# Kernel optimization log

Measured on AMD Instinct MI355X. Metric: run time of the kernel, lower is better.

The kernel has to match this reference:

```python
import jax, jax.numpy as jnp
import numpy as np

B, N, D, K = 16, 65536, 24, 512
ATTRACTION_WEIGHT = 1.0
REPULSION_WEIGHT = 1.5
MARGIN_WEIGHT = 5.0
THRESHOLD = 0.5
MARGIN = 0.2
TAU = 0.7


def setup_inputs() -> dict:
    key = jax.random.key(0)
    k1, k2, k3 = jax.random.split(key, 3)
    beta = jax.random.normal(k1, (B, N, 1), jnp.float32)
    embed = jax.random.normal(k2, (B, N, D), jnp.float32)
    # First K hits of each event are the condensation points (one per instance),
    # remaining hits get a random instance id in [0, K).
    rand_sid = jax.random.randint(k3, (B, N - K), 0, K, jnp.int32)
    cp_sid = jnp.broadcast_to(jnp.arange(K, dtype=jnp.int32), (B, K))
    slice_id = jnp.concatenate([cp_sid, rand_sid], axis=1)
    is_cp = jnp.concatenate(
        [jnp.ones((B, K), jnp.int32), jnp.zeros((B, N - K), jnp.int32)], axis=1)
    return {"beta": beta, "embed": embed, "slice_id": slice_id, "is_cp": is_cp}


def _per_batch(beta_b, emb_b, sid, cp):
    # beta_b: [N], emb_b: [N, D], sid: [N] int, cp: [N] int
    n = beta_b.shape[0]
    f32 = beta_b.dtype
    cp_mask = cp == 1
    pos_count = cp_mask.sum()
    neg_count = n - pos_count

    seg_cnt = jax.ops.segment_sum(jnp.ones((n,), f32), sid, num_segments=K)
    inst_present = seg_cnt > 0
    cp_per_inst = jax.ops.segment_sum(cp_mask.astype(f32), sid, num_segments=K)
    valid_inst = inst_present & (cp_per_inst == 1)  # inst_cp.sum() == 1

    # --- grouped softmax CE over each instance (temperature TAU) ---
    logits = jnp.clip(beta_b, -20.0, 20.0) / TAU
    seg_max = jax.ops.segment_max(logits, sid, num_segments=K)
    safe_max = jnp.where(inst_present, seg_max, 0.0)
    ex = jnp.exp(logits - safe_max[sid])
    denom = jax.ops.segment_sum(ex, sid, num_segments=K)
    cp_logit = jax.ops.segment_sum(jnp.where(cp_mask, logits, 0.0), sid,
                                   num_segments=K)  # exactly one cp when valid
    p_cp = jnp.exp(cp_logit - safe_max) / jnp.maximum(denom, 1e-30)
    loss_inst = -jnp.log(p_cp + 1e-9)
    slice_count = valid_inst.sum()
    beta_slice_ce = jnp.where(valid_inst, loss_inst, 0.0).sum() / jnp.maximum(slice_count, 1)

    # --- margin loss on sigmoid(beta) ---
    beta_prob = jax.nn.sigmoid(jnp.clip(beta_b, -20.0, 20.0))
    pos_m = jnp.where(cp_mask, jax.nn.relu(THRESHOLD + MARGIN - beta_prob), 0.0).sum() \
        / jnp.maximum(pos_count, 1)
    neg_m = jnp.where(cp_mask, 0.0, jax.nn.relu(beta_prob - (THRESHOLD - MARGIN))).sum() \
        / jnp.maximum(neg_count, 1)
    beta_loss = beta_slice_ce + MARGIN_WEIGHT * (pos_m + neg_m)

    # --- attraction: hits pulled to first CP of their instance ---
    idx = jnp.arange(n, dtype=jnp.int32)
    first_cp = jax.ops.segment_min(jnp.where(cp_mask, idx, n), sid, num_segments=K)
    has_cp = (first_cp < n) & inst_present
    cp_emb = emb_b[jnp.minimum(first_cp, n - 1)]  # [K, D]
    d2 = jnp.minimum(((emb_b - cp_emb[sid]) ** 2).sum(-1), 50.0)
    d2_mean = jax.ops.segment_sum(d2, sid, num_segments=K) / jnp.maximum(seg_cnt, 1.0)
    attraction = ATTRACTION_WEIGHT * jnp.where(has_cp, d2_mean, 0.0).sum()

    # --- repulsion: pairwise exp(-d2) between CP embeddings (incl. diagonal) ---
    m = has_cp.astype(f32)
    mcount = m.sum()
    sq = (cp_emb ** 2).sum(-1)
    pd2 = sq[:, None] + sq[None, :] - 2.0 * (cp_emb @ cp_emb.T)
    pd2 = jnp.clip(pd2, 0.0, 50.0)
    rep = (jnp.exp(-pd2) * (m[:, None] * m[None, :])).sum() / jnp.maximum(mcount * mcount, 1.0)
    repulsion = jnp.where(mcount > 1, REPULSION_WEIGHT * rep, 0.0)

    valid = (pos_count >= 1) & (neg_count >= 1) & (slice_count > 0)
    total = beta_loss + attraction + repulsion
    return total, beta_loss, attraction, repulsion, valid


def reference(beta, embed, slice_id, is_cp):
    beta = jnp.nan_to_num(jnp.squeeze(beta, -1), nan=0.0, posinf=0.0, neginf=0.0)
    embed = jnp.nan_to_num(embed, nan=0.0, posinf=0.0, neginf=0.0)
    total, bl, al, rl, valid = jax.vmap(_per_batch)(beta, embed, slice_id, is_cp)
    v = valid.astype(beta.dtype)
    count = v.sum()
    safe = jnp.maximum(count, 1.0)
    ok = count > 0
    final = jnp.where(ok, (total * v).sum() / safe, 0.0)
    beta_log = jnp.where(ok, (bl * v).sum() / safe, 0.0)
    attr_log = jnp.where(ok, (al * v).sum() / safe, 0.0)
    repl_log = jnp.where(ok, (rl * v).sum() / safe, 0.0)
    return final, beta_log, attr_log, repl_log
```

## Files before the change

kernel.cpp:

```cpp
#include <hip/hip_runtime.h>
#include <math.h>

#define BB 16
#define NN 65536
#define DD 24
#define KK 512
#define CH 64
#define HPB (NN / CH)
#define TPB 256
#define RPB 8
#define FIRST_INIT 0x7F7F7F7F

__device__ __forceinline__ float fixnum(float v) {
  return __builtin_isfinite(v) ? v : 0.0f;
}

__device__ __forceinline__ float blockReduceSum(float v, float* sbuf) {
  __syncthreads();
  #pragma unroll
  for (int off = 32; off > 0; off >>= 1) v += __shfl_down(v, off, 64);
  int wid = threadIdx.x >> 6, lane = threadIdx.x & 63;
  if (lane == 0) sbuf[wid] = v;
  __syncthreads();
  return sbuf[0] + sbuf[1] + sbuf[2] + sbuf[3];
}

__global__ __launch_bounds__(TPB) void k1_seg(
    const float* __restrict__ beta, const int* __restrict__ sid,
    const int* __restrict__ iscp,
    float* __restrict__ cnt_g, float* __restrict__ den_g,
    float* __restrict__ cpc_g, float* __restrict__ cpl_g,
    int* __restrict__ first_g, float* __restrict__ marg_g)
{
  __shared__ float s_cnt[KK], s_den[KK], s_cpc[KK], s_cpl[KK];
  __shared__ int   s_first[KK];
  __shared__ float sred[4];
  int b = blockIdx.x >> 6, c = blockIdx.x & 63, t = threadIdx.x;
  for (int k = t; k < KK; k += TPB) {
    s_cnt[k] = 0.f; s_den[k] = 0.f; s_cpc[k] = 0.f; s_cpl[k] = 0.f; s_first[k] = NN;
  }
  __syncthreads();
  int h0 = c * HPB + t * 4;
  size_t g0 = (size_t)b * NN + h0;
  float4 bv = *(const float4*)(beta + g0);
  int4   sv = *(const int4*)(sid + g0);
  int4   cv = *(const int4*)(iscp + g0);
  float pm = 0.f, nm = 0.f;
  float bs[4] = {bv.x, bv.y, bv.z, bv.w};
  int   ss[4] = {sv.x, sv.y, sv.z, sv.w};
  int   cs[4] = {cv.x, cv.y, cv.z, cv.w};
  #pragma unroll
  for (int j = 0; j < 4; ++j) {
    float bc = fminf(fmaxf(fixnum(bs[j]), -20.f), 20.f);
    float logit = bc * (1.0f / 0.7f);
    int s = ss[j];
    atomicAdd(&s_cnt[s], 1.0f);
    atomicAdd(&s_den[s], __expf(logit));
    float prob = 1.0f / (1.0f + __expf(-bc));
    if (cs[j] == 1) {
      atomicAdd(&s_cpc[s], 1.0f);
      atomicAdd(&s_cpl[s], logit);
      atomicMin(&s_first[s], h0 + j);
      pm += fmaxf(0.7f - prob, 0.f);
    } else {
      nm += fmaxf(prob - 0.3f, 0.f);
    }
  }
  float pms = blockReduceSum(pm, sred);
  float nms = blockReduceSum(nm, sred);
  if (t == 0) {
    if (pms != 0.f) atomicAdd(&marg_g[2 * b], pms);
    if (nms != 0.f) atomicAdd(&marg_g[2 * b + 1], nms);
  }
  __syncthreads();
  int base = b * KK;
  for (int k = t; k < KK; k += TPB) {
    if (s_cnt[k] != 0.f) {
      atomicAdd(&cnt_g[base + k], s_cnt[k]);
      atomicAdd(&den_g[base + k], s_den[k]);
    }
    if (s_cpc[k] != 0.f) {
      atomicAdd(&cpc_g[base + k], s_cpc[k]);
      atomicAdd(&cpl_g[base + k], s_cpl[k]);
    }
    if (s_first[k] < NN) atomicMin(&first_g[base + k], s_first[k]);
  }
}

__global__ __launch_bounds__(TPB) void k3_attr_rep(
    const float* __restrict__ embed, const int* __restrict__ sid,
    const int* __restrict__ first_g,
    float* __restrict__ d2_acc, float* __restrict__ rep_acc)
{
  __shared__ float s_tile[64 * 25];
  __shared__ float s_d2[KK];
  __shared__ int   s_first[KK];
  __shared__ float sred[4];
  int b = blockIdx.x >> 6, c = blockIdx.x & 63, t = threadIdx.x;

  for (int k = t; k < KK; k += TPB) {
    s_first[k] = first_g[b * KK + k];
    s_d2[k] = 0.f;
  }

  int hl = t >> 2, q = t & 3, d0 = q * 6;
  int rbase = hl * 25 + d0;
  int wI[3];
  #pragma unroll
  for (int j = 0; j < 3; ++j) {
    int f = 2 * (t + j * TPB);
    int h = f / 24;
    wI[j] = h * 25 + (f - h * 24);
  }

  size_t hit0 = (size_t)b * NN + (size_t)c * HPB;
  const float* embB = embed + (size_t)b * NN * DD;
  const float2* eb2 = (const float2*)(embed + hit0 * DD);
  const int* sidb = sid + hit0;

  float2 r[3];
  #pragma unroll
  for (int j = 0; j < 3; ++j) r[j] = eb2[t + j * TPB];
  __syncthreads();

  for (int tile = 0; tile < 16; ++tile) {
    #pragma unroll
    for (int j = 0; j < 3; ++j) {
      s_tile[wI[j]]     = fixnum(r[j].x);
      s_tile[wI[j] + 1] = fixnum(r[j].y);
    }
    __syncthreads();
    if (tile < 15) {
      const float2* nb = eb2 + (size_t)(tile + 1) * (64 * DD / 2);
      #pragma unroll
      for (int j = 0; j < 3; ++j) r[j] = nb[t + j * TPB];
    }
    int s = sidb[tile * 64 + hl];
    int fs = s_first[s];
    int row = fs < NN ? fs : 0;
    const float2* cep = (const float2*)(embB + (size_t)row * DD + d0);
    float2 c0 = cep[0], c1 = cep[1], c2 = cep[2];
    float ce[6] = {fixnum(c0.x), fixnum(c0.y), fixnum(c1.x),
                   fixnum(c1.y), fixnum(c2.x), fixnum(c2.y)};
    float d2 = 0.f;
    #pragma unroll
    for (int d = 0; d < 6; ++d) {
      float x = s_tile[rbase + d] - ce[d];
      d2 += x * x;
    }
    d2 += __shfl_xor(d2, 1, 64);
    d2 += __shfl_xor(d2, 2, 64);
    if (q == 0) atomicAdd(&s_d2[s], fminf(d2, 50.f));
    __syncthreads();
  }

  for (int k = t; k < KK; k += TPB)
    atomicAdd(&d2_acc[b * KK + k], s_d2[k]);

  int j0 = t, j1 = t + TPB;
  int f0 = s_first[j0], f1 = s_first[j1];
  float m0 = f0 < NN ? 1.f : 0.f, m1 = f1 < NN ? 1.f : 0.f;
  int r0 = f0 < NN ? f0 : 0, r1 = f1 < NN ? f1 : 0;
  float cj0[DD], cj1[DD];
  const float4* cj0p = (const float4*)(embB + (size_t)r0 * DD);
  const float4* cj1p = (const float4*)(embB + (size_t)r1 * DD);
  #pragma unroll
  for (int qq = 0; qq < DD / 4; ++qq) {
    float4 a = cj0p[qq], bq = cj1p[qq];
    cj0[qq*4]   = fixnum(a.x);  cj0[qq*4+1] = fixnum(a.y);
    cj0[qq*4+2] = fixnum(a.z);  cj0[qq*4+3] = fixnum(a.w);
    cj1[qq*4]   = fixnum(bq.x); cj1[qq*4+1] = fixnum(bq.y);
    cj1[qq*4+2] = fixnum(bq.z); cj1[qq*4+3] = fixnum(bq.w);
  }
  float acc = 0.f;
  #pragma unroll
  for (int ri = 0; ri < RPB; ++ri) {
    int i = c * RPB + ri;
    int fi = s_first[i];
    float mi = fi < NN ? 1.f : 0.f;
    const float* rowp = embB + (size_t)(fi < NN ? fi : 0) * DD;
    float d20 = 0.f, d21 = 0.f;
    #pragma unroll
    for (int d = 0; d < DD; ++d) {
      float ci = fixnum(rowp[d]);
      float x0 = ci - cj0[d]; d20 += x0 * x0;
      float x1 = ci - cj1[d]; d21 += x1 * x1;
    }
    acc += mi * (m0 * __expf(-fminf(d20, 50.f)) + m1 * __expf(-fminf(d21, 50.f)));
  }
  float tot = blockReduceSum(acc, sred);
  if (t == 0) atomicAdd(&rep_acc[b], tot);
}

__global__ __launch_bounds__(1024) void k4_final(
    const float* __restrict__ cnt_g, const float* __restrict__ den_g,
    const float* __restrict__ cpc_g, const float* __restrict__ cpl_g,
    const int* __restrict__ first_g, const float* __restrict__ d2_acc,
    const float* __restrict__ marg_g, const float* __restrict__ rep_acc,
    float* __restrict__ out)
{
  __shared__ float s_b[BB][5];
  int w = threadIdx.x >> 6, l = threadIdx.x & 63;
  int b = w;
  float attr = 0.f, ce = 0.f, vcnt = 0.f, pcnt = 0.f, mcnt = 0.f;
  #pragma unroll
  for (int k = l; k < KK; k += 64) {
    int idx = b * KK + k;
    float cnt = cnt_g[idx], den = den_g[idx];
    float cpc = cpc_g[idx], cpl = cpl_g[idx];
    int   fc  = first_g[idx];
    float d2  = d2_acc[idx];
    bool present = cnt > 0.f;
    bool vinst = present && (cpc == 1.0f);
    float p = __expf(cpl) / fmaxf(den, 1e-30f);
    float hc = (fc < NN) ? 1.f : 0.f;
    ce   += vinst ? -__logf(p + 1e-9f) : 0.f;
    attr += hc * (d2 / fmaxf(cnt, 1.f));
    vcnt += vinst ? 1.f : 0.f;
    pcnt += cpc;
    mcnt += hc;
  }
  #pragma unroll
  for (int off = 32; off > 0; off >>= 1) {
    attr += __shfl_down(attr, off, 64);
    ce   += __shfl_down(ce, off, 64);
    vcnt += __shfl_down(vcnt, off, 64);
    pcnt += __shfl_down(pcnt, off, 64);
    mcnt += __shfl_down(mcnt, off, 64);
  }
  if (l == 0) {
    float pm = marg_g[2 * b], nm = marg_g[2 * b + 1];
    float pos = pcnt, neg = (float)NN - pos;
    float slice_ce = ce / fmaxf(vcnt, 1.f);
    float beta_loss = slice_ce + 5.0f * (pm / fmaxf(pos, 1.f) + nm / fmaxf(neg, 1.f));
    float rep = rep_acc[b] / fmaxf(mcnt * mcnt, 1.f);
    float repulsion = (mcnt > 1.f) ? 1.5f * rep : 0.f;
    float v = (pos >= 1.f && neg >= 1.f && vcnt > 0.f) ? 1.f : 0.f;
    s_b[w][0] = (beta_loss + attr + repulsion) * v;
    s_b[w][1] = beta_loss * v;
    s_b[w][2] = attr * v;
    s_b[w][3] = repulsion * v;
    s_b[w][4] = v;
  }
  __syncthreads();
  if (threadIdx.x == 0) {
    float s0 = 0.f, s1 = 0.f, s2 = 0.f, s3 = 0.f, cv = 0.f;
    #pragma unroll
    for (int i = 0; i < BB; ++i) {
      s0 += s_b[i][0]; s1 += s_b[i][1]; s2 += s_b[i][2]; s3 += s_b[i][3]; cv += s_b[i][4];
    }
    float safe = fmaxf(cv, 1.f);
    bool ok = cv > 0.f;
    out[0] = ok ? s0 / safe : 0.f;
    out[1] = ok ? s1 / safe : 0.f;
    out[2] = ok ? s2 / safe : 0.f;
    out[3] = ok ? s3 / safe : 0.f;
  }
}

extern "C" void kernel_launch(void* const* d_in, const int* in_sizes, int n_in,
                              void* d_out, int out_size, void* d_ws, size_t ws_size,
                              hipStream_t stream) {
  (void)in_sizes; (void)n_in; (void)out_size; (void)ws_size;
  const float* beta  = (const float*)d_in[0];
  const float* embed = (const float*)d_in[1];
  const int*   sid   = (const int*)d_in[2];
  const int*   iscp  = (const int*)d_in[3];
  float* out = (float*)d_out;
  char* ws = (char*)d_ws;

  size_t off = 0;
  auto alloc = [&](size_t bytes) {
    size_t o = off; off += (bytes + 255) & ~(size_t)255; return o;
  };
  const size_t BKf = (size_t)BB * KK * 4;
  size_t o_zero  = alloc(0);
  size_t o_cnt   = alloc(BKf);
  size_t o_den   = alloc(BKf);
  size_t o_cpc   = alloc(BKf);
  size_t o_cpl   = alloc(BKf);
  size_t o_d2    = alloc(BKf);
  size_t o_marg  = alloc((size_t)BB * 2 * 4);
  size_t o_rep   = alloc((size_t)BB * 4);
  size_t zbytes  = off - o_zero;
  size_t o_first = alloc(BKf);

  float* p_cnt  = (float*)(ws + o_cnt);
  float* p_den  = (float*)(ws + o_den);
  float* p_cpc  = (float*)(ws + o_cpc);
  float* p_cpl  = (float*)(ws + o_cpl);
  float* p_d2   = (float*)(ws + o_d2);
  float* p_marg = (float*)(ws + o_marg);
  float* p_rep  = (float*)(ws + o_rep);
  int*   p_fst  = (int*)(ws + o_first);

  hipMemsetAsync(ws + o_zero, 0, zbytes, stream);
  hipMemsetAsync(ws + o_first, 0x7F, BKf, stream);

  k1_seg<<<BB * CH, TPB, 0, stream>>>(beta, sid, iscp,
      p_cnt, p_den, p_cpc, p_cpl, p_fst, p_marg);

  k3_attr_rep<<<BB * CH, TPB, 0, stream>>>(embed, sid, p_fst, p_d2, p_rep);

  k4_final<<<1, 1024, 0, stream>>>(p_cnt, p_den, p_cpc, p_cpl,
      p_fst, p_d2, p_marg, p_rep, out);
}
```

Baseline: 210.5 us.

## Double-buffer attraction tiles and double the k3 grid with fewer tiles per block

```diff
diff --git a/kernel.cpp b/kernel.cpp
--- a/kernel.cpp
+++ b/kernel.cpp
@@ -8,8 +8,9 @@
 #define CH 64
 #define HPB (NN / CH)
 #define TPB 256
-#define RPB 8
-#define FIRST_INIT 0x7F7F7F7F
+#define CH3 128
+#define HPB3 (NN / CH3)
+#define RPB3 4
 
 __device__ __forceinline__ float fixnum(float v) {
   return __builtin_isfinite(v) ? v : 0.0f;
@@ -92,16 +93,24 @@
     const int* __restrict__ first_g,
     float* __restrict__ d2_acc, float* __restrict__ rep_acc)
 {
-  __shared__ float s_tile[64 * 25];
+  __shared__ float s_tile[2][64 * 25];
   __shared__ float s_d2[KK];
   __shared__ int   s_first[KK];
+  __shared__ int   s_sid[HPB3];
   __shared__ float sred[4];
-  int b = blockIdx.x >> 6, c = blockIdx.x & 63, t = threadIdx.x;
+  int b = blockIdx.x >> 7, c = blockIdx.x & 127, t = threadIdx.x;
+
+  size_t hit0 = (size_t)b * NN + (size_t)c * HPB3;
+  const float* embB = embed + (size_t)b * NN * DD;
+  const float2* eb2 = (const float2*)(embed + hit0 * DD);
+  const int* sidb = sid + hit0;
 
   for (int k = t; k < KK; k += TPB) {
     s_first[k] = first_g[b * KK + k];
     s_d2[k] = 0.f;
   }
+  s_sid[t] = sidb[t];
+  s_sid[t + TPB] = sidb[t + TPB];
 
   int hl = t >> 2, q = t & 3, d0 = q * 6;
   int rbase = hl * 25 + d0;
@@ -113,49 +122,61 @@
     wI[j] = h * 25 + (f - h * 24);
   }
 
-  size_t hit0 = (size_t)b * NN + (size_t)c * HPB;
-  const float* embB = embed + (size_t)b * NN * DD;
-  const float2* eb2 = (const float2*)(embed + hit0 * DD);
-  const int* sidb = sid + hit0;
-
   float2 r[3];
   #pragma unroll
   for (int j = 0; j < 3; ++j) r[j] = eb2[t + j * TPB];
   __syncthreads();
 
-  for (int tile = 0; tile < 16; ++tile) {
-    #pragma unroll
-    for (int j = 0; j < 3; ++j) {
-      s_tile[wI[j]]     = fixnum(r[j].x);
-      s_tile[wI[j] + 1] = fixnum(r[j].y);
-    }
+  int scur = s_sid[hl];
+  int fc0 = s_first[scur];
+  int rw0 = fc0 < NN ? fc0 : 0;
+  const float2* cp0 = (const float2*)(embB + (size_t)rw0 * DD + d0);
+  float2 cc0 = cp0[0], cc1 = cp0[1], cc2 = cp0[2];
+  #pragma unroll
+  for (int j = 0; j < 3; ++j) {
+    s_tile[0][wI[j]]     = fixnum(r[j].x);
+    s_tile[0][wI[j] + 1] = fixnum(r[j].y);
+  }
+
+  #pragma unroll
+  for (int tile = 0; tile < 8; ++tile) {
     __syncthreads();
-    if (tile < 15) {
+    int cur = tile & 1;
+    int snext = 0;
+    float2 cn0 = {0.f, 0.f}, cn1 = {0.f, 0.f}, cn2 = {0.f, 0.f};
+    if (tile < 7) {
       const float2* nb = eb2 + (size_t)(tile + 1) * (64 * DD / 2);
-      #pragma unroll
-      for (int j = 0; j < 3; ++j) r[j] = nb[t + j * TPB];
-    }
-    int s = sidb[tile * 64 + hl];
-    int fs = s_first[s];
-    int row = fs < NN ? fs : 0;
-    const float2* cep = (const float2*)(embB + (size_t)row * DD + d0);
-    float2 c0 = cep[0], c1 = cep[1], c2 = cep[2];
-    float ce[6] = {fixnum(c0.x), fixnum(c0.y), fixnum(c1.x),
-                   fixnum(c1.y), fixnum(c2.x), fixnum(c2.y)};
-    float d2 = 0.f;
-    #pragma unroll
-    for (int d = 0; d < 6; ++d) {
-      float x = s_tile[rbase + d] - ce[d];
-      d2 += x * x;
-    }
+      r[0] = nb[t]; r[1] = nb[t + TPB]; r[2] = nb[t + 2 * TPB];
+      snext = s_sid[(tile + 1) * 64 + hl];
+      int fn = s_first[snext];
+      int rn = fn < NN ? fn : 0;
+      const float2* cpn = (const float2*)(embB + (size_t)rn * DD + d0);
+      cn0 = cpn[0]; cn1 = cpn[1]; cn2 = cpn[2];
+    }
+    float e0 = fixnum(cc0.x), e1 = fixnum(cc0.y), e2 = fixnum(cc1.x),
+          e3 = fixnum(cc1.y), e4 = fixnum(cc2.x), e5 = fixnum(cc2.y);
+    float d2 = 0.f, x;
+    x = s_tile[cur][rbase + 0] - e0; d2 += x * x;
+    x = s_tile[cur][rbase + 1] - e1; d2 += x * x;
+    x = s_tile[cur][rbase + 2] - e2; d2 += x * x;
+    x = s_tile[cur][rbase + 3] - e3; d2 += x * x;
+    x = s_tile[cur][rbase + 4] - e4; d2 += x * x;
+    x = s_tile[cur][rbase + 5] - e5; d2 += x * x;
     d2 += __shfl_xor(d2, 1, 64);
     d2 += __shfl_xor(d2, 2, 64);
-    if (q == 0) atomicAdd(&s_d2[s], fminf(d2, 50.f));
-    __syncthreads();
-  }
-
+    if (q == 0) atomicAdd(&s_d2[scur], fminf(d2, 50.f));
+    if (tile < 7) {
+      #pragma unroll
+      for (int j = 0; j < 3; ++j) {
+        s_tile[cur ^ 1][wI[j]]     = fixnum(r[j].x);
+        s_tile[cur ^ 1][wI[j] + 1] = fixnum(r[j].y);
+      }
+      scur = snext; cc0 = cn0; cc1 = cn1; cc2 = cn2;
+    }
+  }
+  __syncthreads();
   for (int k = t; k < KK; k += TPB)
-    atomicAdd(&d2_acc[b * KK + k], s_d2[k]);
+    if (s_d2[k] != 0.f) atomicAdd(&d2_acc[b * KK + k], s_d2[k]);
 
   int j0 = t, j1 = t + TPB;
   int f0 = s_first[j0], f1 = s_first[j1];
@@ -174,8 +195,8 @@
   }
   float acc = 0.f;
   #pragma unroll
-  for (int ri = 0; ri < RPB; ++ri) {
-    int i = c * RPB + ri;
+  for (int ri = 0; ri < RPB3; ++ri) {
+    int i = c * RPB3 + ri;
     int fi = s_first[i];
     float mi = fi < NN ? 1.f : 0.f;
     const float* rowp = embB + (size_t)(fi < NN ? fi : 0) * DD;
@@ -300,7 +321,7 @@
   k1_seg<<<BB * CH, TPB, 0, stream>>>(beta, sid, iscp,
       p_cnt, p_den, p_cpc, p_cpl, p_fst, p_marg);
 
-  k3_attr_rep<<<BB * CH, TPB, 0, stream>>>(embed, sid, p_fst, p_d2, p_rep);
+  k3_attr_rep<<<BB * CH3, TPB, 0, stream>>>(embed, sid, p_fst, p_d2, p_rep);
 
   k4_final<<<1, 1024, 0, stream>>>(p_cnt, p_den, p_cpc, p_cpl,
       p_fst, p_d2, p_marg, p_rep, out);
```

Measured after the change: 207.6 us. Within noise of the previous version (-1.3%).
